# Kernel optimization log

Measured on AMD Instinct MI355X. Metric: run time of the kernel, lower is better.

## Reference

```python
import jax, jax.numpy as jnp
import numpy as np

NUM_EMBEDDINGS = 8192
EMBEDDING_DIM = 256
BETA = 0.25


def setup_inputs() -> dict:
    key = jax.random.key(0)
    k1, k2 = jax.random.split(key)
    z = jax.random.normal(k1, (16, 256, 32, 32), dtype=jnp.float32)
    # torch init: uniform(-1/K, 1/K)
    emb_w = jax.random.uniform(k2, (NUM_EMBEDDINGS, EMBEDDING_DIM),
                               dtype=jnp.float32,
                               minval=-1.0 / NUM_EMBEDDINGS,
                               maxval=1.0 / NUM_EMBEDDINGS)
    return {"z": z, "emb_w": emb_w}


def reference(z, emb_w):
    B, C, H, W = z.shape
    z_bhwc = jnp.transpose(z, (0, 2, 3, 1))          # [B,H,W,C]
    flat = z_bhwc.reshape(-1, C)                      # [N,C]
    d = (jnp.sum(flat * flat, axis=1, keepdims=True)
         + jnp.sum(emb_w * emb_w, axis=1)
         - 2.0 * flat @ emb_w.T)                      # [N,K]
    idx = jnp.argmin(d, axis=1)                       # [N]
    # direct gather (mathematically identical to one-hot @ emb_w)
    quantized = emb_w[idx].reshape(z_bhwc.shape)      # [B,H,W,C]
    q_latent_loss = jnp.mean((jax.lax.stop_gradient(quantized) - z_bhwc) ** 2)
    e_latent_loss = jnp.mean((quantized - jax.lax.stop_gradient(z_bhwc)) ** 2)
    loss = q_latent_loss + BETA * e_latent_loss
    # straight-through estimator
    quantized_st = z_bhwc + jax.lax.stop_gradient(quantized - z_bhwc)
    out = jnp.transpose(quantized_st, (0, 3, 1, 2))   # [B,C,H,W]
    return out, loss, idx.reshape(B, -1)
```

## Files before the change

kernel.cpp:

```cpp
#include <hip/hip_runtime.h>
#include <cstdint>
#include <cstddef>

#define N_PIX   16384
#define K_EMB   8192
#define DDIM    256

#define WS_A8       0
#define WS_E8       4194304
#define WS_KEYS     6291456
#define WS_ZSQ      23068672
#define WS_ESQ      23134208
#define WS_LOSS     23166976
#define WS_CNT      23166984

typedef float f32x4 __attribute__((ext_vector_type(4)));

__device__ __forceinline__ unsigned int f32_sortable(float f) {
    unsigned int u = __float_as_uint(f);
    return (u & 0x80000000u) ? ~u : (u | 0x80000000u);
}

__device__ __forceinline__ unsigned char f2fp8(float x) {
    unsigned ub = __float_as_uint(x);
    unsigned sgn = (ub >> 24) & 0x80u;
    unsigned b = ub & 0x7FFFFFFFu;
    unsigned out;
    if (__uint_as_float(b) < 0.015625f) {
        out = (unsigned)(int)rintf(__uint_as_float(b) * 512.0f);
    } else {
        unsigned r = b + 0x7FFFFu + ((b >> 20) & 1u);
        int er = (int)(r >> 23) - 127;
        out = (unsigned)(((er + 7) << 3) | ((r >> 20) & 7u));
    }
    return (unsigned char)(out | sgn);
}

#if defined(__has_builtin)
#if __has_builtin(__builtin_amdgcn_cvt_pk_fp8_f32)
#define HAVE_CVT_FP8 1
#endif
#if __has_builtin(__builtin_amdgcn_fmed3f)
#define HAVE_FMED3 1
#endif
#endif

__device__ __forceinline__ unsigned pack4_fp8(float a, float b, float c, float d) {
#ifdef HAVE_CVT_FP8
    int pk = 0;
    pk = __builtin_amdgcn_cvt_pk_fp8_f32(a, b, pk, false);
    pk = __builtin_amdgcn_cvt_pk_fp8_f32(c, d, pk, true);
    return (unsigned)pk;
#else
    return (unsigned)f2fp8(a) | ((unsigned)f2fp8(b) << 8)
         | ((unsigned)f2fp8(c) << 16) | ((unsigned)f2fp8(d) << 24);
#endif
}

__device__ __forceinline__ void async16(const unsigned char* g, unsigned char* l) {
    __builtin_amdgcn_global_load_lds(
        (const __attribute__((address_space(1))) void*)g,
        (__attribute__((address_space(3))) void*)l, 16, 0, 0);
}

__device__ __forceinline__ float np_pairwise_sq256(const float* row) {
    float r[16];
#pragma unroll
    for (int j = 0; j < 16; ++j) r[j] = 0.f;
#pragma unroll
    for (int c = 0; c < 256; ++c) {
        float x  = row[c];
        float sq = __fmul_rn(x, x);
        int slot = ((c >> 7) << 3) | (c & 7);
        r[slot] = __fadd_rn(r[slot], sq);
    }
    float h0 = __fadd_rn(
        __fadd_rn(__fadd_rn(r[0], r[1]), __fadd_rn(r[2], r[3])),
        __fadd_rn(__fadd_rn(r[4], r[5]), __fadd_rn(r[6], r[7])));
    float h1 = __fadd_rn(
        __fadd_rn(__fadd_rn(r[8], r[9]), __fadd_rn(r[10], r[11])),
        __fadd_rn(__fadd_rn(r[12], r[13]), __fadd_rn(r[14], r[15])));
    return __fadd_rn(h0, h1);
}

__device__ __forceinline__ size_t cm_addr(int r, int c) {
    int ks = c >> 5;
    int h  = (c >> 4) & 1;
    int s  = h ^ ((r >> 2) & 1);
    return (size_t)ks * 4096 + (size_t)r * 32 + s * 16 + (c & 15);
}

__global__ __launch_bounds__(256) void prep_kernel(
        const float* __restrict__ z, const float* __restrict__ emb,
        unsigned char* __restrict__ Af8, unsigned char* __restrict__ Ef8,
        float* __restrict__ zsq, float* __restrict__ esq,
        double* __restrict__ lossAcc, unsigned* __restrict__ doneCnt) {
    __shared__ float tile[32][257];
    int blk = blockIdx.x;
    int t   = threadIdx.x;
    if (blk < 512) {
        int b   = blk >> 5;
        int hw0 = (blk & 31) * 32;
        const float* zb = z + (size_t)b * 262144 + hw0;
        int c0  = t >> 3;
        int px4 = t & 7;
#pragma unroll
        for (int cc = 0; cc < 8; ++cc) {
            int c = cc * 32 + c0;
            float4 v = *(const float4*)&zb[(size_t)c * 1024 + px4 * 4];
            tile[px4 * 4 + 0][c] = v.x;
            tile[px4 * 4 + 1][c] = v.y;
            tile[px4 * 4 + 2][c] = v.z;
            tile[px4 * 4 + 3][c] = v.w;
        }
        __syncthreads();
        int p0 = b * 1024 + hw0;
        int wv = t >> 6, lane = t & 63;
#pragma unroll
        for (int iter = 0; iter < 8; ++iter) {
            int pl = iter * 4 + wv;
            unsigned pk = pack4_fp8(tile[pl][lane * 4 + 0], tile[pl][lane * 4 + 1],
                                    tile[pl][lane * 4 + 2], tile[pl][lane * 4 + 3]);
            int p  = p0 + pl;
            int mb = p >> 7, r = p & 127;
            *(unsigned*)(Af8 + (size_t)mb * 32768 + cm_addr(r, lane * 4)) = pk;
        }
        if (t < 32) zsq[p0 + t] = np_pairwise_sq256(tile[t]);
        if (blk == 0 && t == 0) { *lossAcc = 0.0; *doneCnt = 0u; }
    } else {
        int k0 = (blk - 512) * 32;
        const float4* eg = (const float4*)(emb + (size_t)k0 * DDIM);
#pragma unroll
        for (int i = 0; i < 8; ++i) {
            int idx = i * 256 + t;
            int row = idx >> 6, c4 = idx & 63;
            float4 v = eg[idx];
            *(float4*)&tile[row][c4 * 4] = v;
        }
        __syncthreads();
#pragma unroll
        for (int i = 0; i < 8; ++i) {
            int idx = i * 256 + t;
            int row = idx >> 6, c4 = idx & 63;
            const float* rp = &tile[row][c4 * 4];
            int kg = k0 + row;
            int nb = kg >> 7, rr = kg & 127;
            *(unsigned*)(Ef8 + (size_t)nb * 32768 + cm_addr(rr, c4 * 4)) =
                pack4_fp8(rp[0] * 8192.0f, rp[1] * 8192.0f,
                          rp[2] * 8192.0f, rp[3] * 8192.0f);
        }
        if (t < 32) esq[k0 + t] = np_pairwise_sq256(tile[t]);
    }
}

__device__ __forceinline__ unsigned pack_key(float w) {
    float uf = __builtin_fmaf(w, -512.0f, 262144.0f);
    uf = fminf(uf, 524287.0f);
    unsigned u = (unsigned)uf;
    return (u << 13) | (__float_as_uint(w) & 0x1FFFu);
}

__global__ __launch_bounds__(256) void mfma_score_kernel(
        const unsigned char* __restrict__ Af8,
        const unsigned char* __restrict__ Ef8,
        unsigned int* __restrict__ keys) {
    union SM {
        unsigned char Bs[2][8][4096];
        struct { uint2 ep[128][33]; } e;
    };
    __shared__ SM sm;

    const int g  = blockIdx.x;
    const int mb = blockIdx.y;
    const int t = threadIdx.x;
    const int w = t >> 6, lane = t & 63;
    const int wm = w >> 1, wn = w & 1;
    const int quad = lane >> 4, l16 = lane & 15;

    {
        const unsigned char* Eg = Ef8 + (size_t)(g * 4) * 32768 + t * 16;
#pragma unroll
        for (int ks = 0; ks < 8; ++ks)
            async16(Eg + ks * 4096, &sm.Bs[0][ks][t * 16]);
    }

    int aaddr[4], baddr[4];
#pragma unroll
    for (int fi = 0; fi < 4; ++fi) {
        int row = wm * 64 + fi * 16 + l16;
        int gg  = (quad >> 1) ^ ((row >> 2) & 1);
        aaddr[fi] = row * 32 + gg * 16 + (quad & 1) * 8;
    }
#pragma unroll
    for (int fj = 0; fj < 4; ++fj) {
        int row = wn * 64 + fj * 16 + l16;
        int gg  = (quad >> 1) ^ ((row >> 2) & 1);
        baddr[fj] = row * 32 + gg * 16 + (quad & 1) * 8;
    }

    long long afr[4][8];
    {
        const unsigned char* Agb = Af8 + (size_t)mb * 32768;
#pragma unroll
        for (int fi = 0; fi < 4; ++fi)
#pragma unroll
            for (int ks = 0; ks < 8; ++ks)
                afr[fi][ks] = *(const long long*)(Agb + ks * 4096 + aaddr[fi]);
    }

    const float NEGINF = __int_as_float(0xFF800000);
    float t2a[16], t2b[16];
#pragma unroll
    for (int i = 0; i < 16; ++i) { t2a[i] = NEGINF; t2b[i] = NEGINF; }

    __syncthreads();

#pragma unroll 1
    for (int j = 0; j < 4; ++j) {
        const int cur = j & 1, nxt = cur ^ 1;

        if (j < 3) {
            const unsigned char* Egn =
                Ef8 + (size_t)(g * 4 + j + 1) * 32768 + t * 16;
#pragma unroll
            for (int ks = 0; ks < 8; ++ks)
                async16(Egn + ks * 4096, &sm.Bs[nxt][ks][t * 16]);
        }

        f32x4 acc[4][4];
#pragma unroll
        for (int i = 0; i < 4; ++i)
#pragma unroll
            for (int jj = 0; jj < 4; ++jj)
#pragma unroll
                for (int r = 0; r < 4; ++r) acc[i][jj][r] = 0.f;

#pragma unroll
        for (int ks = 0; ks < 8; ++ks) {
            long long bfr[4];
#pragma unroll
            for (int fj = 0; fj < 4; ++fj)
                bfr[fj] = *(const long long*)&sm.Bs[cur][ks][baddr[fj]];
            __builtin_amdgcn_s_setprio(1);
#pragma unroll
            for (int fi = 0; fi < 4; ++fi)
#pragma unroll
                for (int fj = 0; fj < 4; ++fj)
                    acc[fi][fj] = __builtin_amdgcn_mfma_f32_16x16x32_fp8_fp8(
                        afr[fi][ks], bfr[fj], acc[fi][fj], 0, 0, 0);
            __builtin_amdgcn_s_setprio(0);
        }

        const int nb = g * 4 + j;
        const unsigned idx0 = (unsigned)(nb * 128 + wn * 64 + l16);
#pragma unroll
        for (int fi = 0; fi < 4; ++fi) {
#pragma unroll
            for (int r = 0; r < 4; ++r) {
                const int ai = fi * 4 + r;
                float a0 = t2a[ai], b0 = t2b[ai];
#pragma unroll
                for (int fj = 0; fj < 4; ++fj) {
                    float v = acc[fi][fj][r];
                    float wv = __uint_as_float(
                        (__float_as_uint(v) & 0xFFFFE000u) | (idx0 + fj * 16));
#ifdef HAVE_FMED3
                    float bn = __builtin_amdgcn_fmed3f(a0, wv, b0);
                    a0 = fmaxf(a0, wv);
                    b0 = bn;
#else
                    float mn = fminf(a0, wv);
                    a0 = fmaxf(a0, wv);
                    b0 = fmaxf(b0, mn);
#endif
                }
                t2a[ai] = a0; t2b[ai] = b0;
            }
        }
        __syncthreads();
    }

#pragma unroll
    for (int fi = 0; fi < 4; ++fi) {
#pragma unroll
        for (int r = 0; r < 4; ++r) {
            const int ai = fi * 4 + r;
            int row = wm * 64 + fi * 16 + quad * 4 + r;
            sm.e.ep[row][wn * 16 + l16] =
                make_uint2(pack_key(t2a[ai]), pack_key(t2b[ai]));
        }
    }
    __syncthreads();

    {
        int row = t >> 1, half = t & 1, h0 = half * 16;
        uint2 mv = sm.e.ep[row][h0];
#pragma unroll
        for (int i = 1; i < 16; ++i) {
            uint2 av = sm.e.ep[row][h0 + i];
            unsigned n0 = min(mv.x, av.x);
            unsigned n1 = min(max(mv.x, av.x), min(mv.y, av.y));
            mv.x = n0; mv.y = n1;
        }
        ((uint2*)keys)[(size_t)(g * 2 + half) * N_PIX + (mb * 128 + row)] = mv;
    }
}

__global__ __launch_bounds__(256) void final_kernel(
        const unsigned int* __restrict__ keys,
        const float* __restrict__ z, const float* __restrict__ emb,
        const float* __restrict__ zsq, const float* __restrict__ esq,
        float* __restrict__ out, float* __restrict__ idx_out,
        float* __restrict__ loss_out,
        double* __restrict__ lossAcc, unsigned* __restrict__ doneCnt) {
    __shared__ float ztile[16][260];
    __shared__ uint2 kt[16][33];
    __shared__ int   scand[16][64];
    __shared__ unsigned long long ckey[1024];
    __shared__ int   soff[17];
    __shared__ int   scnt[16];
    __shared__ int   pxmap[1024];
    __shared__ float szs[16];
    __shared__ int   sidx[16];

    int blk = blockIdx.x;
    int b = blk >> 6, hh = blk & 63;
    int t = threadIdx.x;
    int p0 = b * 1024 + hh * 16;
    const float* zb = z + (size_t)b * 262144 + hh * 16;
    {
        int px = t & 15, cb = t >> 4;
#pragma unroll
        for (int cc = 0; cc < 16; ++cc) {
            int c = cc * 16 + cb;
            ztile[px][c] = zb[(size_t)c * 1024 + px];
        }
    }
    {
        const uint2* kg = (const uint2*)keys;
#pragma unroll
        for (int itr = 0; itr < 2; ++itr) {
            int idx = itr * 256 + t;
            int px = idx & 15, hf = idx >> 4;
            kt[px][hf] = kg[(size_t)hf * N_PIX + p0 + px];
        }
    }
    if (t < 16) szs[t] = zsq[p0 + t];
    __syncthreads();

    {
        int wq = t >> 6, lane = t & 63;
#pragma unroll 1
        for (int i = 0; i < 4; ++i) {
            int px = wq * 4 + i;
            uint2 ka = (lane < 32) ? kt[px][lane] : make_uint2(~0u, ~0u);
            unsigned m = min(ka.x, ka.y);
#pragma unroll
            for (int off = 32; off >= 1; off >>= 1)
                m = min(m, (unsigned)__shfl_xor((int)m, off, 64));
            unsigned thr = (m >> 13) + 1600;

            bool h0 = (lane < 32) && ((ka.x >> 13) <= thr);
            bool h1 = (lane < 32) && ((ka.y >> 13) <= thr);
            unsigned long long m0 = __ballot(h0);
            unsigned long long m1 = __ballot(h1);
            int c0 = __popcll(m0);
            unsigned long long below = (lane == 63) ? ~0ull >> 1
                                     : ((1ull << lane) - 1);
            if (h0) scand[px][__popcll(m0 & below)] = (int)(ka.x & 0x1FFFu);
            if (h1) scand[px][c0 + __popcll(m1 & below)] = (int)(ka.y & 0x1FFFu);
            if (lane == 0) scnt[px] = c0 + __popcll(m1);
        }
    }
    __syncthreads();

    if (t < 64) {
        int v = (t < 16) ? scnt[t] : 0;
#pragma unroll
        for (int o = 1; o < 16; o <<= 1) {
            int u = __shfl_up(v, o, 64);
            if (t >= o) v += u;
        }
        if (t < 16) soff[t + 1] = v;
        if (t == 0) soff[0] = 0;
    }
    __syncthreads();
    int total = soff[16];
    for (int f = t; f < total; f += 256) {
        int lo = 0, hi = 15;
        while (lo < hi) {
            int mid = (lo + hi + 1) >> 1;
            if (soff[mid] <= f) lo = mid; else hi = mid - 1;
        }
        pxmap[f] = lo;
    }
    __syncthreads();

    {
        int gid = t >> 4, l16 = t & 15;
        const float4* emb4 = (const float4*)emb;
#pragma unroll 1
        for (int f = gid; f < total; f += 16) {
            int px = pxmap[f];
            int k  = scand[px][f - soff[px]];
            double d = 0.0;
#pragma unroll
            for (int q = 0; q < 4; ++q) {
                float4 ev = emb4[(size_t)k * 64 + q * 16 + l16];
                const float* zp = &ztile[px][(q * 16 + l16) * 4];
                d += (double)zp[0] * ev.x + (double)zp[1] * ev.y
                   + (double)zp[2] * ev.z + (double)zp[3] * ev.w;
            }
#pragma unroll
            for (int o = 1; o < 16; o <<= 1) d += __shfl_xor(d, o, 64);
            if (l16 == 0) {
                float df = (float)d;
                float s  = __fsub_rn(__fadd_rn(szs[px], esq[k]),
                                     __fmul_rn(2.0f, df));
                ckey[f] = ((unsigned long long)f32_sortable(s) << 32)
                        | (unsigned)k;
            }
        }
    }
    __syncthreads();

    {
        int cpx = t >> 4, ci = t & 15;
        unsigned long long best = ~0ull;
        for (int f = soff[cpx] + ci; f < soff[cpx + 1]; f += 16) {
            unsigned long long v = ckey[f];
            best = v < best ? v : best;
        }
#pragma unroll
        for (int o = 1; o < 16; o <<= 1) {
            unsigned long long ov =
                (unsigned long long)__shfl_xor((long long)best, o, 64);
            best = ov < best ? ov : best;
        }
        if (ci == 0) {
            int k = (int)(unsigned)(best & 0xffffffffu);
            sidx[cpx] = k;
            idx_out[p0 + cpx] = (float)k;
        }
    }
    __syncthreads();

    int px2 = t & 15, cy = t >> 4;
    int kk = sidx[px2];
    const float* er = emb + (size_t)kk * DDIM;
    float* ob = out + (size_t)b * 262144 + hh * 16;
    float local = 0.f;
#pragma unroll 4
    for (int it = 0; it < 16; ++it) {
        int c = it * 16 + cy;
        float q = er[c];
        float d = q - ztile[px2][c];
        ob[(size_t)c * 1024 + px2] = q;
        local += d * d;
    }
#pragma unroll
    for (int off = 32; off >= 1; off >>= 1) local += __shfl_down(local, off, 64);
    __shared__ float wsum[4];
    if ((t & 63) == 0) wsum[t >> 6] = local;
    __syncthreads();
    if (t == 0) {
        double s = (double)wsum[0] + (double)wsum[1]
                 + (double)wsum[2] + (double)wsum[3];
        atomicAdd(lossAcc, s);
        __threadfence();
        unsigned old = atomicAdd(doneCnt, 1u);
        if (old == 1023u) {
            double tot = atomicAdd(lossAcc, 0.0);
            *loss_out = (float)(tot * (1.25 / 4194304.0));
        }
    }
}

extern "C" void kernel_launch(void* const* d_in, const int* in_sizes, int n_in,
                              void* d_out, int out_size, void* d_ws, size_t ws_size,
                              hipStream_t stream) {
    const float* z   = (const float*)d_in[0];
    const float* emb = (const float*)d_in[1];
    float* out = (float*)d_out;
    char* ws = (char*)d_ws;

    unsigned char* Af8 = (unsigned char*)(ws + WS_A8);
    unsigned char* Ef8 = (unsigned char*)(ws + WS_E8);
    unsigned int* keys = (unsigned int*)(ws + WS_KEYS);
    float* zsq      = (float*)(ws + WS_ZSQ);
    float* esq      = (float*)(ws + WS_ESQ);
    double* lossAcc = (double*)(ws + WS_LOSS);
    unsigned* doneCnt = (unsigned*)(ws + WS_CNT);

    prep_kernel<<<768, 256, 0, stream>>>(z, emb, Af8, Ef8, zsq, esq,
                                         lossAcc, doneCnt);
    mfma_score_kernel<<<dim3(16, 128), 256, 0, stream>>>(Af8, Ef8, keys);
    final_kernel<<<1024, 256, 0, stream>>>(keys, z, emb, zsq, esq,
                                           out, out + 4194305, out + 4194304,
                                           lossAcc, doneCnt);
}
```

Measured before the change: 190.8 us.

## Switch score GEMM to 32x32x64 scaled FP8 MFMA with new operand layout

```diff
diff --git a/kernel.cpp b/kernel.cpp
--- a/kernel.cpp
+++ b/kernel.cpp
@@ -14,7 +14,9 @@
 #define WS_LOSS     23166976
 #define WS_CNT      23166984
 
-typedef float f32x4 __attribute__((ext_vector_type(4)));
+typedef float f32x16 __attribute__((ext_vector_type(16)));
+typedef int   i32x4  __attribute__((ext_vector_type(4)));
+typedef int   i32x8  __attribute__((ext_vector_type(8)));
 
 __device__ __forceinline__ unsigned int f32_sortable(float f) {
     unsigned int u = __float_as_uint(f);
@@ -81,13 +83,6 @@
         __fadd_rn(__fadd_rn(r[8], r[9]), __fadd_rn(r[10], r[11])),
         __fadd_rn(__fadd_rn(r[12], r[13]), __fadd_rn(r[14], r[15])));
     return __fadd_rn(h0, h1);
-}
-
-__device__ __forceinline__ size_t cm_addr(int r, int c) {
-    int ks = c >> 5;
-    int h  = (c >> 4) & 1;
-    int s  = h ^ ((r >> 2) & 1);
-    return (size_t)ks * 4096 + (size_t)r * 32 + s * 16 + (c & 15);
 }
 
 __global__ __launch_bounds__(256) void prep_kernel(
@@ -122,8 +117,10 @@
             unsigned pk = pack4_fp8(tile[pl][lane * 4 + 0], tile[pl][lane * 4 + 1],
                                     tile[pl][lane * 4 + 2], tile[pl][lane * 4 + 3]);
             int p  = p0 + pl;
-            int mb = p >> 7, r = p & 127;
-            *(unsigned*)(Af8 + (size_t)mb * 32768 + cm_addr(r, lane * 4)) = pk;
+            int mbb = p >> 7, r = p & 127;
+            int c = lane * 4;
+            *(unsigned*)(Af8 + (size_t)mbb * 32768
+                         + (c >> 6) * 8192 + r * 64 + (c & 63)) = pk;
         }
         if (t < 32) zsq[p0 + t] = np_pairwise_sq256(tile[t]);
         if (blk == 0 && t == 0) { *lossAcc = 0.0; *doneCnt = 0u; }
@@ -144,8 +141,13 @@
             int row = idx >> 6, c4 = idx & 63;
             const float* rp = &tile[row][c4 * 4];
             int kg = k0 + row;
-            int nb = kg >> 7, rr = kg & 127;
-            *(unsigned*)(Ef8 + (size_t)nb * 32768 + cm_addr(rr, c4 * 4)) =
+            int nbb = kg >> 7, rr = kg & 127;
+            int c  = c4 * 4;
+            int kk = c >> 6, kl = c & 63;
+            int s  = kl >> 4;
+            int pos = kk * 8192 + rr * 64
+                    + ((s ^ ((rr >> 1) & 3)) << 4) + (kl & 15);
+            *(unsigned*)(Ef8 + (size_t)nbb * 32768 + pos) =
                 pack4_fp8(rp[0] * 8192.0f, rp[1] * 8192.0f,
                           rp[2] * 8192.0f, rp[3] * 8192.0f);
         }
@@ -164,8 +166,8 @@
         const unsigned char* __restrict__ Af8,
         const unsigned char* __restrict__ Ef8,
         unsigned int* __restrict__ keys) {
-    union SM {
-        unsigned char Bs[2][8][4096];
+    union __align__(16) SM {
+        unsigned char Bs[2][32768];
         struct { uint2 ep[128][33]; } e;
     };
     __shared__ SM sm;
@@ -175,43 +177,38 @@
     const int t = threadIdx.x;
     const int w = t >> 6, lane = t & 63;
     const int wm = w >> 1, wn = w & 1;
-    const int quad = lane >> 4, l16 = lane & 15;
+    const int l31 = lane & 31, h = lane >> 5;
 
     {
         const unsigned char* Eg = Ef8 + (size_t)(g * 4) * 32768 + t * 16;
 #pragma unroll
-        for (int ks = 0; ks < 8; ++ks)
-            async16(Eg + ks * 4096, &sm.Bs[0][ks][t * 16]);
-    }
-
-    int aaddr[4], baddr[4];
-#pragma unroll
-    for (int fi = 0; fi < 4; ++fi) {
-        int row = wm * 64 + fi * 16 + l16;
-        int gg  = (quad >> 1) ^ ((row >> 2) & 1);
-        aaddr[fi] = row * 32 + gg * 16 + (quad & 1) * 8;
-    }
-#pragma unroll
-    for (int fj = 0; fj < 4; ++fj) {
-        int row = wn * 64 + fj * 16 + l16;
-        int gg  = (quad >> 1) ^ ((row >> 2) & 1);
-        baddr[fj] = row * 32 + gg * 16 + (quad & 1) * 8;
-    }
-
-    long long afr[4][8];
-    {
-        const unsigned char* Agb = Af8 + (size_t)mb * 32768;
-#pragma unroll
-        for (int fi = 0; fi < 4; ++fi)
-#pragma unroll
-            for (int ks = 0; ks < 8; ++ks)
-                afr[fi][ks] = *(const long long*)(Agb + ks * 4096 + aaddr[fi]);
+        for (int ch = 0; ch < 8; ++ch)
+            async16(Eg + ch * 4096, &sm.Bs[0][ch * 4096 + t * 16]);
+    }
+
+    i32x8 afr[2][4];
+    {
+        const unsigned char* Ab = Af8 + (size_t)mb * 32768;
+#pragma unroll
+        for (int rt = 0; rt < 2; ++rt) {
+            int r = wm * 64 + rt * 32 + l31;
+#pragma unroll
+            for (int kk = 0; kk < 4; ++kk) {
+                const unsigned char* p = Ab + kk * 8192 + r * 64 + h * 32;
+                i32x4 lo = *(const i32x4*)p;
+                i32x4 hi = *(const i32x4*)(p + 16);
+                afr[rt][kk] = __builtin_shufflevector(lo, hi,
+                                                      0, 1, 2, 3, 4, 5, 6, 7);
+            }
+        }
     }
 
     const float NEGINF = __int_as_float(0xFF800000);
-    float t2a[16], t2b[16];
-#pragma unroll
-    for (int i = 0; i < 16; ++i) { t2a[i] = NEGINF; t2b[i] = NEGINF; }
+    float t2a[2][16], t2b[2][16];
+#pragma unroll
+    for (int rt = 0; rt < 2; ++rt)
+#pragma unroll
+        for (int q = 0; q < 16; ++q) { t2a[rt][q] = NEGINF; t2b[rt][q] = NEGINF; }
 
     __syncthreads();
 
@@ -220,74 +217,92 @@
         const int cur = j & 1, nxt = cur ^ 1;
 
         if (j < 3) {
-            const unsigned char* Egn =
+            const unsigned char* Eg =
                 Ef8 + (size_t)(g * 4 + j + 1) * 32768 + t * 16;
 #pragma unroll
-            for (int ks = 0; ks < 8; ++ks)
-                async16(Egn + ks * 4096, &sm.Bs[nxt][ks][t * 16]);
-        }
-
-        f32x4 acc[4][4];
-#pragma unroll
-        for (int i = 0; i < 4; ++i)
-#pragma unroll
-            for (int jj = 0; jj < 4; ++jj)
-#pragma unroll
-                for (int r = 0; r < 4; ++r) acc[i][jj][r] = 0.f;
-
-#pragma unroll
-        for (int ks = 0; ks < 8; ++ks) {
-            long long bfr[4];
-#pragma unroll
-            for (int fj = 0; fj < 4; ++fj)
-                bfr[fj] = *(const long long*)&sm.Bs[cur][ks][baddr[fj]];
+            for (int ch = 0; ch < 8; ++ch)
+                async16(Eg + ch * 4096, &sm.Bs[nxt][ch * 4096 + t * 16]);
+        }
+
+        f32x16 acc[2][2];
+#pragma unroll
+        for (int rt = 0; rt < 2; ++rt)
+#pragma unroll
+            for (int ct = 0; ct < 2; ++ct)
+#pragma unroll
+                for (int q = 0; q < 16; ++q) acc[rt][ct][q] = 0.f;
+
+#pragma unroll
+        for (int kk = 0; kk < 4; ++kk) {
+            i32x8 bf[2];
+#pragma unroll
+            for (int ct = 0; ct < 2; ++ct) {
+                int c = wn * 64 + ct * 32 + l31;
+                int m = (c >> 1) & 3;
+                int base = kk * 8192 + c * 64;
+                int s0 = h * 2;
+                i32x4 lo = *(const i32x4*)
+                    &sm.Bs[cur][base + ((s0 ^ m) << 4)];
+                i32x4 hi = *(const i32x4*)
+                    &sm.Bs[cur][base + (((s0 + 1) ^ m) << 4)];
+                bf[ct] = __builtin_shufflevector(lo, hi,
+                                                 0, 1, 2, 3, 4, 5, 6, 7);
+            }
             __builtin_amdgcn_s_setprio(1);
 #pragma unroll
-            for (int fi = 0; fi < 4; ++fi)
-#pragma unroll
-                for (int fj = 0; fj < 4; ++fj)
-                    acc[fi][fj] = __builtin_amdgcn_mfma_f32_16x16x32_fp8_fp8(
-                        afr[fi][ks], bfr[fj], acc[fi][fj], 0, 0, 0);
+            for (int rt = 0; rt < 2; ++rt)
+#pragma unroll
+                for (int ct = 0; ct < 2; ++ct)
+                    acc[rt][ct] =
+                        __builtin_amdgcn_mfma_scale_f32_32x32x64_f8f6f4(
+                            afr[rt][kk], bf[ct], acc[rt][ct],
+                            0, 0,
+                            0, 0x7F7F7F7F,
+                            0, 0x7F7F7F7F);
             __builtin_amdgcn_s_setprio(0);
         }
 
         const int nb = g * 4 + j;
-        const unsigned idx0 = (unsigned)(nb * 128 + wn * 64 + l16);
-#pragma unroll
-        for (int fi = 0; fi < 4; ++fi) {
-#pragma unroll
-            for (int r = 0; r < 4; ++r) {
-                const int ai = fi * 4 + r;
-                float a0 = t2a[ai], b0 = t2b[ai];
-#pragma unroll
-                for (int fj = 0; fj < 4; ++fj) {
-                    float v = acc[fi][fj][r];
+#pragma unroll
+        for (int ct = 0; ct < 2; ++ct) {
+            const unsigned idxc = (unsigned)(nb * 128 + wn * 64 + ct * 32 + l31);
+#pragma unroll
+            for (int rt = 0; rt < 2; ++rt) {
+#pragma unroll
+                for (int q = 0; q < 16; ++q) {
+                    float v = acc[rt][ct][q];
                     float wv = __uint_as_float(
-                        (__float_as_uint(v) & 0xFFFFE000u) | (idx0 + fj * 16));
+                        (__float_as_uint(v) & 0xFFFFE000u) | idxc);
+                    float a0 = t2a[rt][q], b0 = t2b[rt][q];
 #ifdef HAVE_FMED3
                     float bn = __builtin_amdgcn_fmed3f(a0, wv, b0);
-                    a0 = fmaxf(a0, wv);
-                    b0 = bn;
+                    t2a[rt][q] = fmaxf(a0, wv);
+                    t2b[rt][q] = bn;
 #else
                     float mn = fminf(a0, wv);
-                    a0 = fmaxf(a0, wv);
-                    b0 = fmaxf(b0, mn);
+                    t2a[rt][q] = fmaxf(a0, wv);
+                    t2b[rt][q] = fmaxf(b0, mn);
 #endif
                 }
-                t2a[ai] = a0; t2b[ai] = b0;
             }
         }
         __syncthreads();
     }
 
 #pragma unroll
-    for (int fi = 0; fi < 4; ++fi) {
-#pragma unroll
-        for (int r = 0; r < 4; ++r) {
-            const int ai = fi * 4 + r;
-            int row = wm * 64 + fi * 16 + quad * 4 + r;
-            sm.e.ep[row][wn * 16 + l16] =
-                make_uint2(pack_key(t2a[ai]), pack_key(t2b[ai]));
+    for (int rt = 0; rt < 2; ++rt) {
+#pragma unroll
+        for (int q = 0; q < 16; ++q) {
+            unsigned ka = pack_key(t2a[rt][q]);
+            unsigned kb = pack_key(t2b[rt][q]);
+            unsigned pa = (unsigned)__shfl_xor((int)ka, 16, 64);
+            unsigned pb = (unsigned)__shfl_xor((int)kb, 16, 64);
+            unsigned n0 = min(ka, pa);
+            unsigned n1 = min(max(ka, pa), min(kb, pb));
+            if ((lane & 16) == 0) {
+                int row = wm * 64 + rt * 32 + (q & 3) + 8 * (q >> 2) + 4 * h;
+                sm.e.ep[row][wn * 16 + (lane & 15)] = make_uint2(n0, n1);
+            }
         }
     }
     __syncthreads();
```

Result: no change. 187.1 us (-1.9%).
